# Optimization experiments

Hardware: AMD Instinct MI355X
Metric: run time of the kernel (lower is better)

The kernel has to match this reference:

```python
import jax, jax.numpy as jnp
import numpy as np

SAMPLING_RATE = 48000
HARMONIC_NUM = 8
DIM = HARMONIC_NUM + 1
SINE_AMP = 0.1
NOISE_STD = 0.003
VOICED_THRESHOLD = 0.0


def setup_inputs() -> dict:
    key = jax.random.key(0)
    B, T = 4, 480000
    # realistic voiced pitch contour in [80, 400) Hz
    f0 = jax.random.uniform(key, (B, T, 1), dtype=jnp.float32, minval=80.0, maxval=400.0)
    return {"f0": f0}


def reference(f0):
    B, T, _ = f0.shape
    # harmonic stack: f0_buf[:, :, k] = f0 * (k+1)   -> [B, T, DIM]
    harmonics = jnp.arange(1, DIM + 1, dtype=f0.dtype)
    f0_buf = f0 * harmonics  # broadcast [B,T,1] * [DIM]

    # normalized phase increment per sample
    rad_values = (f0_buf / SAMPLING_RATE) % 1.0

    # random initial phase per (batch, harmonic); fundamental gets phase 0
    k_ini, k_noise = jax.random.split(jax.random.key(42))
    rand_ini = jax.random.uniform(k_ini, (B, DIM), dtype=f0.dtype)
    rand_ini = rand_ini.at[:, 0].set(0.0)
    rad_values = rad_values.at[:, 0, :].add(rand_ini)

    # phase-unwrap correction: detect wrap points of cumsum % 1 and subtract 1
    tmp_over_one = jnp.cumsum(rad_values, axis=1) % 1.0
    wrap = (tmp_over_one[:, 1:, :] - tmp_over_one[:, :-1, :]) < 0  # [B,T-1,DIM]
    cumsum_shift = jnp.concatenate(
        [jnp.zeros((B, 1, DIM), dtype=f0.dtype), -wrap.astype(f0.dtype)], axis=1
    )

    phase = jnp.cumsum(rad_values + cumsum_shift, axis=1) * (2.0 * jnp.pi)
    sine_waves = jnp.sin(phase) * SINE_AMP  # [B,T,DIM]

    # voiced/unvoiced mask from fundamental f0
    uv = (f0 > VOICED_THRESHOLD).astype(f0.dtype)  # [B,T,1]

    noise_amp = uv * NOISE_STD + (1.0 - uv) * (SINE_AMP / 3.0)
    noise = jax.random.normal(k_noise, sine_waves.shape, dtype=f0.dtype)
    return sine_waves * uv + noise_amp * noise
```

## Files before the change

kernel.cpp:

```cpp
#include <hip/hip_runtime.h>
#include <math.h>
#include <stdint.h>

#pragma clang fp contract(off)

#define BB   4
#define TT   480000
#define DIM  9
#define TILE 256
#define NTT  1875

#define PARTITIONABLE 1

__host__ __device__ static inline void threefry2x32(uint32_t k0, uint32_t k1,
                                                    uint32_t x0, uint32_t x1,
                                                    uint32_t& o0, uint32_t& o1) {
  const uint32_t ks2 = k0 ^ k1 ^ 0x1BD11BDAu;
  x0 += k0; x1 += k1;
#define TF_R(r) { x0 += x1; x1 = (x1 << (r)) | (x1 >> (32 - (r))); x1 ^= x0; }
  TF_R(13) TF_R(15) TF_R(26) TF_R(6)
  x0 += k1;  x1 += ks2 + 1u;
  TF_R(17) TF_R(29) TF_R(16) TF_R(24)
  x0 += ks2; x1 += k0 + 2u;
  TF_R(13) TF_R(15) TF_R(26) TF_R(6)
  x0 += k0;  x1 += k1 + 3u;
  TF_R(17) TF_R(29) TF_R(16) TF_R(24)
  x0 += k1;  x1 += ks2 + 4u;
  TF_R(13) TF_R(15) TF_R(26) TF_R(6)
  x0 += ks2; x1 += k0 + 5u;
#undef TF_R
  o0 = x0; o1 = x1;
}

__device__ __forceinline__ float fracf_(float x) { return x - truncf(x); }

__device__ __forceinline__ float u01_(uint32_t bits) {
  return __uint_as_float((bits >> 9) | 0x3f800000u) - 1.0f;
}

__device__ static inline float erfinv_xla(float x) {
  float t = (1.0f - x) * (1.0f + x);
  float w = -0.6931471805599453f * __builtin_amdgcn_logf(t);
  float p;
  if (w < 5.0f) {
    w = w - 2.5f;
    p = 2.81022636e-08f;
    p = 3.43273939e-07f  + p * w;
    p = -3.5233877e-06f  + p * w;
    p = -4.39150654e-06f + p * w;
    p = 0.00021858087f   + p * w;
    p = -0.00125372503f  + p * w;
    p = -0.00417768164f  + p * w;
    p = 0.246640727f     + p * w;
    p = 1.50140941f      + p * w;
  } else {
    w = __builtin_amdgcn_sqrtf(w) - 3.0f;
    p = -0.000200214257f;
    p = 0.000100950558f  + p * w;
    p = 0.00134934322f   + p * w;
    p = -0.00367342844f  + p * w;
    p = 0.00573950773f   + p * w;
    p = -0.0076224613f   + p * w;
    p = 0.00943887047f   + p * w;
    p = 1.00167406f      + p * w;
    p = 2.83297682f      + p * w;
  }
  return p * x;
}

__device__ __forceinline__ float nrm_(uint32_t bits) {
  const float LO = -0.9999999403953552f;
  float u = u01_(bits) * 2.0f + LO;
  u = fmaxf(LO, u);
  return 1.4142135623730951f * erfinv_xla(u);
}

__device__ __forceinline__ uint32_t ri_bits(uint32_t kk0, uint32_t kk1, uint32_t j) {
  uint32_t o0, o1;
#if PARTITIONABLE
  threefry2x32(kk0, kk1, 0u, j, o0, o1);
  return o0 ^ o1;
#else
  if (j < 18u) { threefry2x32(kk0, kk1, j, j + 18u, o0, o1); return o0; }
  threefry2x32(kk0, kk1, j - 18u, j, o0, o1); return o1;
#endif
}

__device__ __forceinline__ uint32_t noise_bits(uint32_t kn0, uint32_t kn1, uint32_t i) {
  uint32_t o0, o1;
#if PARTITIONABLE
  threefry2x32(kn0, kn1, 0u, i, o0, o1);
  return o0 ^ o1;
#else
  const uint32_t half = 2u * TT * DIM;
  if (i < half) { threefry2x32(kn0, kn1, i, i + half, o0, o1); return o0; }
  threefry2x32(kn0, kn1, i - half, i, o0, o1); return o1;
#endif
}

__device__ __forceinline__ float rand_ini_val(uint32_t ki0, uint32_t ki1, int b, int k) {
  if (k == 0) return 0.0f;
  return u01_(ri_bits(ki0, ki1, (uint32_t)(b * DIM + k)));
}

__device__ __forceinline__ float selbit(unsigned long long m, float aFalse, float bTrue) {
  float r;
  asm("v_cndmask_b32 %0, %1, %2, %3" : "=v"(r) : "v"(aFalse), "v"(bTrue), "s"(m));
  return r;
}

struct Tree { float n1a, n1b, Mv[6]; };

__device__ __forceinline__ void build_tree4(float x0, float x1, float x2, float x3,
                                            Tree& T, int l) {
  T.n1a = x0 + x1;
  T.n1b = x2 + x3;
  T.Mv[0] = T.n1a + T.n1b;
#pragma unroll
  for (int s = 1; s < 6; ++s)
    T.Mv[s] = __shfl(T.Mv[s - 1], 2 * l) + __shfl(T.Mv[s - 1], 2 * l + 1);
}
__device__ __forceinline__ float tile_sum4(const Tree& T) {
  return __shfl(T.Mv[5], 0) + __shfl(T.Mv[5], 1);
}
__device__ __forceinline__ float fold4(const Tree& T, int n, float carry) {
  float acc = carry;
#pragma unroll
  for (int b = 7; b >= 2; --b) {
    float t = __shfl(T.Mv[b - 2], (n >> (b + 1)) << 1);
    acc = ((n >> b) & 1) ? acc + t : acc;
  }
  if (n & 2) acc = acc + T.n1a;
  return acc;
}

__global__ __launch_bounds__(256) void k_up1(const float* __restrict__ f0,
                                             float* __restrict__ gL,
                                             uint32_t ki0, uint32_t ki1) {
  int task = blockIdx.x * 4 + (threadIdx.x >> 6);
  int l = threadIdx.x & 63;
  int b = task / NTT, j = task - b * NTT;
  float4 f4 = *(const float4*)(f0 + (size_t)b * TT + j * TILE + 4 * l);
  const float RINV = 1.0f / 48000.0f;
  float rb0 = f4.x * RINV, rb1 = f4.y * RINV, rb2 = f4.z * RINV, rb3 = f4.w * RINV;
  bool ini = (j == 0) & (l == 0);
#pragma unroll
  for (int k = 0; k < DIM; ++k) {
    float h = (float)(k + 1);
    float r0 = fracf_(rb0 * h), r1 = fracf_(rb1 * h);
    float r2 = fracf_(rb2 * h), r3 = fracf_(rb3 * h);
    if (ini) r0 = r0 + rand_ini_val(ki0, ki1, b, k);
    Tree T; build_tree4(r0, r1, r2, r3, T, l);
    float ts = tile_sum4(T);
    if (l == 0) gL[(b * DIM + k) * NTT + j] = ts;
  }
}

__global__ __launch_bounds__(256) void k_midscan(float* __restrict__ gbuf) {
  const int NLEV = 11;
  const int SZ[11]  = {1875, 937, 468, 234, 117, 58, 29, 14, 7, 3, 1};
  const int OFF[11] = {0, 1875, 2812, 3280, 3514, 3631, 3689, 3718, 3732, 3739, 3742};
  __shared__ float buf[4][3743];
  int w = threadIdx.x >> 6, l = threadIdx.x & 63;
  int row = blockIdx.x * 4 + w;
  float* g = gbuf + (size_t)row * NTT;
  float* s = buf[w];
  for (int i = l; i < NTT; i += 64) s[i] = g[i];
#pragma unroll
  for (int lv = 0; lv + 1 < NLEV; ++lv) {
    int m = SZ[lv + 1];
    const float* src = s + OFF[lv];
    float* dst = s + OFF[lv + 1];
    for (int i = l; i < m; i += 64) dst[i] = src[2 * i] + src[2 * i + 1];
  }
#pragma unroll
  for (int lv = NLEV - 2; lv >= 0; --lv) {
    int n = SZ[lv], m = SZ[lv + 1];
    float* cur = s + OFF[lv];
    const float* up = s + OFF[lv + 1];
    for (int i = l; i < m; i += 64) {
      float ss = up[i];
      cur[2 * i + 1] = ss;
      if (2 * i + 2 < n) cur[2 * i + 2] = ss + cur[2 * i + 2];
    }
  }
  for (int i = l; i < NTT; i += 64) g[i] = s[i];
}

__global__ __launch_bounds__(256) void k_d1u2(const float* __restrict__ f0,
                                              const float* __restrict__ gS1,
                                              float* __restrict__ gL2,
                                              ulonglong2* __restrict__ wrapw,
                                              uint32_t ki0, uint32_t ki1) {
  int task = blockIdx.x * 4 + (threadIdx.x >> 6);
  int l = threadIdx.x & 63;
  int b = task / NTT, j = task - b * NTT;
  float4 f4 = *(const float4*)(f0 + (size_t)b * TT + j * TILE + 4 * l);
  const float RINV = 1.0f / 48000.0f;
  float rb0 = f4.x * RINV, rb1 = f4.y * RINV, rb2 = f4.z * RINV, rb3 = f4.w * RINV;
  bool ini = (j == 0) & (l == 0);
  bool notfirst = (j > 0) | (l > 0);
#pragma unroll
  for (int k = 0; k < DIM; ++k) {
    float h = (float)(k + 1);
    float r0 = fracf_(rb0 * h), r1 = fracf_(rb1 * h);
    float r2 = fracf_(rb2 * h), r3 = fracf_(rb3 * h);
    if (ini) r0 = r0 + rand_ini_val(ki0, ki1, b, k);
    Tree T; build_tree4(r0, r1, r2, r3, T, l);
    int bju = __builtin_amdgcn_readfirstlane((b * DIM + k) * NTT + j);
    float S = gS1[bju];
    float C = (j > 0) ? gS1[bju - 1] : 0.0f;
    float c3 = fold4(T, 4 * l + 4, C);
    c3 = (l == 63) ? S : c3;
    float c1 = fold4(T, 4 * l + 2, C);
    float cp = __shfl_up(c3, 1);
    if (l == 0) cp = C;
    float c0 = cp + r0;
    float c2 = c1 + r2;
    float fp = fracf_(cp), g0 = fracf_(c0), g1 = fracf_(c1);
    float g2 = fracf_(c2), g3 = fracf_(c3);
    bool w0 = notfirst & (g0 < fp);
    bool w1 = g1 < g0;
    bool w2 = g2 < g1;
    bool w3 = g3 < g2;
    float y0 = w0 ? r0 - 1.0f : r0, y1 = w1 ? r1 - 1.0f : r1;
    float y2 = w2 ? r2 - 1.0f : r2, y3 = w3 ? r3 - 1.0f : r3;
    unsigned long long m0 = __ballot(w0), m1 = __ballot(w1);
    unsigned long long m2 = __ballot(w2), m3 = __ballot(w3);
    Tree Ty; build_tree4(y0, y1, y2, y3, Ty, l);
    float ts = tile_sum4(Ty);
    if (l == 0) {
      gL2[bju] = ts;
      wrapw[2 * (size_t)bju]     = make_ulonglong2(m0, m1);
      wrapw[2 * (size_t)bju + 1] = make_ulonglong2(m2, m3);
    }
  }
}

__global__ __launch_bounds__(256) void k_d2out(const float* __restrict__ f0,
                                               const float* __restrict__ gS2,
                                               const ulonglong2* __restrict__ wrapw,
                                               float* __restrict__ out,
                                               uint32_t ki0, uint32_t ki1,
                                               uint32_t kn0, uint32_t kn1) {
  __shared__ float sb[4][64 * 37];
  int w = threadIdx.x >> 6, l = threadIdx.x & 63;
  int task = blockIdx.x * 4 + w;
  int b = task / NTT, j = task - b * NTT;
  int t0 = j * TILE + 4 * l;
  float4 f4 = *(const float4*)(f0 + (size_t)b * TT + t0);
  const float RINV = 1.0f / 48000.0f;
  float rb0 = f4.x * RINV, rb1 = f4.y * RINV, rb2 = f4.z * RINV, rb3 = f4.w * RINV;
  bool ini = (j == 0) & (l == 0);
  float uv0 = (f4.x > 0.0f) ? 1.0f : 0.0f, uv1 = (f4.y > 0.0f) ? 1.0f : 0.0f;
  float uv2 = (f4.z > 0.0f) ? 1.0f : 0.0f, uv3 = (f4.w > 0.0f) ? 1.0f : 0.0f;
  const float AMP3 = 0.0333333333333333333f;
  float na0 = uv0 * 0.003f + (1.0f - uv0) * AMP3;
  float na1 = uv1 * 0.003f + (1.0f - uv1) * AMP3;
  float na2 = uv2 * 0.003f + (1.0f - uv2) * AMP3;
  float na3 = uv3 * 0.003f + (1.0f - uv3) * AMP3;
  float* sl = sb[w];
  int sbase = l * 37;
#pragma unroll
  for (int k = 0; k < DIM; ++k) {
    float h = (float)(k + 1);
    float r0 = fracf_(rb0 * h), r1 = fracf_(rb1 * h);
    float r2 = fracf_(rb2 * h), r3 = fracf_(rb3 * h);
    if (ini) r0 = r0 + rand_ini_val(ki0, ki1, b, k);
    int bju = __builtin_amdgcn_readfirstlane((b * DIM + k) * NTT + j);
    ulonglong2 wA = wrapw[2 * (size_t)bju];
    ulonglong2 wB = wrapw[2 * (size_t)bju + 1];
    float S2 = gS2[bju];
    float C2 = (j > 0) ? gS2[bju - 1] : 0.0f;
    float y0 = selbit(wA.x, r0, r0 - 1.0f);
    float y1 = selbit(wA.y, r1, r1 - 1.0f);
    float y2 = selbit(wB.x, r2, r2 - 1.0f);
    float y3 = selbit(wB.y, r3, r3 - 1.0f);
    Tree T; build_tree4(y0, y1, y2, y3, T, l);
    float d3 = fold4(T, 4 * l + 4, C2);
    d3 = (l == 63) ? S2 : d3;
    float d1 = fold4(T, 4 * l + 2, C2);
    float dp = __shfl_up(d3, 1);
    if (l == 0) dp = C2;
    float d0 = dp + y0;
    float d2 = d1 + y2;
    float s0 = __builtin_amdgcn_sinf(d0) * 0.1f;
    float s1 = __builtin_amdgcn_sinf(d1) * 0.1f;
    float s2 = __builtin_amdgcn_sinf(d2) * 0.1f;
    float s3 = __builtin_amdgcn_sinf(d3) * 0.1f;
    uint32_t fi = (uint32_t)(b * TT + t0) * (uint32_t)DIM + (uint32_t)k;
    float n0 = nrm_(noise_bits(kn0, kn1, fi));
    float n1 = nrm_(noise_bits(kn0, kn1, fi + 9u));
    float n2 = nrm_(noise_bits(kn0, kn1, fi + 18u));
    float n3 = nrm_(noise_bits(kn0, kn1, fi + 27u));
    sl[sbase + k]      = s0 * uv0 + na0 * n0;
    sl[sbase + 9 + k]  = s1 * uv1 + na1 * n1;
    sl[sbase + 18 + k] = s2 * uv2 + na2 * n2;
    sl[sbase + 27 + k] = s3 * uv3 + na3 * n3;
  }
  float4* po = (float4*)(out + ((size_t)b * TT + (size_t)j * TILE) * DIM);
#pragma unroll
  for (int q = 0; q < 9; ++q) {
    int gg = (q * 64 + l) * 4;
    int a = gg + gg / 36;
    float4 v = make_float4(sl[a], sl[a + 1], sl[a + 2], sl[a + 3]);
    po[q * 64 + l] = v;
  }
}

extern "C" void kernel_launch(void* const* d_in, const int* in_sizes, int n_in,
                              void* d_out, int out_size, void* d_ws, size_t ws_size,
                              hipStream_t stream) {
  (void)in_sizes; (void)n_in; (void)out_size; (void)ws_size;
  const float* f0 = (const float*)d_in[0];
  float* out = (float*)d_out;
  float* gBuf1 = (float*)d_ws;
  float* gBuf2 = gBuf1 + 36 * NTT;
  ulonglong2* wrapw =
      (ulonglong2*)((char*)d_ws + (size_t)2 * 36 * NTT * sizeof(float));

  uint32_t ki0, ki1, kn0, kn1;
#if PARTITIONABLE
  threefry2x32(0u, 42u, 0u, 0u, ki0, ki1);
  threefry2x32(0u, 42u, 0u, 1u, kn0, kn1);
#else
  uint32_t a0, a1, b0, b1;
  threefry2x32(0u, 42u, 0u, 2u, a0, a1);
  threefry2x32(0u, 42u, 1u, 3u, b0, b1);
  ki0 = a0; ki1 = b0;
  kn0 = a1; kn1 = b1;
#endif

  k_up1    <<<(BB * NTT) / 4, 256, 0, stream>>>(f0, gBuf1, ki0, ki1);
  k_midscan<<<9, 256, 0, stream>>>(gBuf1);
  k_d1u2   <<<(BB * NTT) / 4, 256, 0, stream>>>(f0, gBuf1, gBuf2, wrapw, ki0, ki1);
  k_midscan<<<9, 256, 0, stream>>>(gBuf2);
  k_d2out  <<<(BB * NTT) / 4, 256, 0, stream>>>(f0, gBuf2, wrapw, out,
                                                ki0, ki1, kn0, kn1);
}
```

Baseline: 179.3 us.

## Parallelize midscan across 36 blocks and cache per-lane prefix sums for output pass

The middle scan kernel now uses one 256-thread block per row (36 blocks) instead of one wavefront per row in 9 blocks, with block-wide barriers between tree levels. The second downsweep kernel also stores each lane's inclusive partial sum to a workspace buffer. A new output kernel reads those sums instead of rebuilding the tree and folding the prefix. This trades extra global memory traffic (64 floats per tile per harmonic) for less recomputation, and only runs if the workspace is large enough.

```diff
diff --git a/kernel.cpp b/kernel.cpp
--- a/kernel.cpp
+++ b/kernel.cpp
@@ -160,37 +160,44 @@
   const int NLEV = 11;
   const int SZ[11]  = {1875, 937, 468, 234, 117, 58, 29, 14, 7, 3, 1};
   const int OFF[11] = {0, 1875, 2812, 3280, 3514, 3631, 3689, 3718, 3732, 3739, 3742};
-  __shared__ float buf[4][3743];
-  int w = threadIdx.x >> 6, l = threadIdx.x & 63;
-  int row = blockIdx.x * 4 + w;
-  float* g = gbuf + (size_t)row * NTT;
-  float* s = buf[w];
-  for (int i = l; i < NTT; i += 64) s[i] = g[i];
+  __shared__ float buf[3743];
+  float* g = gbuf + (size_t)blockIdx.x * NTT;
+  int tid = threadIdx.x;
+  float tmp[8];
+#pragma unroll
+  for (int u = 0; u < 8; ++u) { int i = tid + u * 256; tmp[u] = (i < NTT) ? g[i] : 0.0f; }
+#pragma unroll
+  for (int u = 0; u < 8; ++u) { int i = tid + u * 256; if (i < NTT) buf[i] = tmp[u]; }
+  __syncthreads();
 #pragma unroll
   for (int lv = 0; lv + 1 < NLEV; ++lv) {
     int m = SZ[lv + 1];
-    const float* src = s + OFF[lv];
-    float* dst = s + OFF[lv + 1];
-    for (int i = l; i < m; i += 64) dst[i] = src[2 * i] + src[2 * i + 1];
+    const float* src = buf + OFF[lv];
+    float* dst = buf + OFF[lv + 1];
+    for (int i = tid; i < m; i += 256) dst[i] = src[2 * i] + src[2 * i + 1];
+    __syncthreads();
   }
 #pragma unroll
   for (int lv = NLEV - 2; lv >= 0; --lv) {
     int n = SZ[lv], m = SZ[lv + 1];
-    float* cur = s + OFF[lv];
-    const float* up = s + OFF[lv + 1];
-    for (int i = l; i < m; i += 64) {
-      float ss = up[i];
-      cur[2 * i + 1] = ss;
-      if (2 * i + 2 < n) cur[2 * i + 2] = ss + cur[2 * i + 2];
+    float* cur = buf + OFF[lv];
+    const float* up = buf + OFF[lv + 1];
+    for (int i = tid; i < m; i += 256) {
+      float s = up[i];
+      cur[2 * i + 1] = s;
+      if (2 * i + 2 < n) cur[2 * i + 2] = s + cur[2 * i + 2];
     }
-  }
-  for (int i = l; i < NTT; i += 64) g[i] = s[i];
+    __syncthreads();
+  }
+#pragma unroll
+  for (int u = 0; u < 8; ++u) { int i = tid + u * 256; if (i < NTT) g[i] = buf[i]; }
 }
 
 __global__ __launch_bounds__(256) void k_d1u2(const float* __restrict__ f0,
                                               const float* __restrict__ gS1,
                                               float* __restrict__ gL2,
                                               ulonglong2* __restrict__ wrapw,
+                                              float* __restrict__ q0buf, int useq,
                                               uint32_t ki0, uint32_t ki1) {
   int task = blockIdx.x * 4 + (threadIdx.x >> 6);
   int l = threadIdx.x & 63;
@@ -229,11 +236,83 @@
     unsigned long long m2 = __ballot(w2), m3 = __ballot(w3);
     Tree Ty; build_tree4(y0, y1, y2, y3, Ty, l);
     float ts = tile_sum4(Ty);
+    if (useq) {
+      float q0 = (l == 63) ? ts : fold4(Ty, 4 * l + 4, 0.0f);
+      q0buf[(size_t)bju * 64 + l] = q0;
+    }
     if (l == 0) {
       gL2[bju] = ts;
       wrapw[2 * (size_t)bju]     = make_ulonglong2(m0, m1);
       wrapw[2 * (size_t)bju + 1] = make_ulonglong2(m2, m3);
     }
+  }
+}
+
+__global__ __launch_bounds__(256) void k_d2out_q(const float* __restrict__ f0,
+                                                 const float* __restrict__ gS2,
+                                                 const ulonglong2* __restrict__ wrapw,
+                                                 const float* __restrict__ q0buf,
+                                                 float* __restrict__ out,
+                                                 uint32_t ki0, uint32_t ki1,
+                                                 uint32_t kn0, uint32_t kn1) {
+  __shared__ float sb[4][64 * 37];
+  int w = threadIdx.x >> 6, l = threadIdx.x & 63;
+  int task = blockIdx.x * 4 + w;
+  int b = task / NTT, j = task - b * NTT;
+  int t0 = j * TILE + 4 * l;
+  float4 f4 = *(const float4*)(f0 + (size_t)b * TT + t0);
+  const float RINV = 1.0f / 48000.0f;
+  float rb0 = f4.x * RINV, rb1 = f4.y * RINV, rb2 = f4.z * RINV;
+  bool ini = (j == 0) & (l == 0);
+  float uv0 = (f4.x > 0.0f) ? 1.0f : 0.0f, uv1 = (f4.y > 0.0f) ? 1.0f : 0.0f;
+  float uv2 = (f4.z > 0.0f) ? 1.0f : 0.0f, uv3 = (f4.w > 0.0f) ? 1.0f : 0.0f;
+  const float AMP3 = 0.0333333333333333333f;
+  float na0 = uv0 * 0.003f + (1.0f - uv0) * AMP3;
+  float na1 = uv1 * 0.003f + (1.0f - uv1) * AMP3;
+  float na2 = uv2 * 0.003f + (1.0f - uv2) * AMP3;
+  float na3 = uv3 * 0.003f + (1.0f - uv3) * AMP3;
+  float* sl = sb[w];
+  int sbase = l * 37;
+#pragma unroll
+  for (int k = 0; k < DIM; ++k) {
+    float h = (float)(k + 1);
+    float r0 = fracf_(rb0 * h), r1 = fracf_(rb1 * h), r2 = fracf_(rb2 * h);
+    if (ini) r0 = r0 + rand_ini_val(ki0, ki1, b, k);
+    int bju = __builtin_amdgcn_readfirstlane((b * DIM + k) * NTT + j);
+    ulonglong2 wA = wrapw[2 * (size_t)bju];
+    unsigned long long wBx = wrapw[2 * (size_t)bju + 1].x;
+    float C2 = (j > 0) ? gS2[bju - 1] : 0.0f;
+    float qv = q0buf[(size_t)bju * 64 + l];
+    float qp = __shfl_up(qv, 1);
+    if (l == 0) qp = 0.0f;
+    float y0 = selbit(wA.x, r0, r0 - 1.0f);
+    float y1 = selbit(wA.y, r1, r1 - 1.0f);
+    float y2 = selbit(wBx, r2, r2 - 1.0f);
+    float base = C2 + qp;
+    float d0 = base + y0;
+    float d1 = base + (y0 + y1);
+    float d2 = d1 + y2;
+    float d3 = C2 + qv;
+    float s0 = __builtin_amdgcn_sinf(d0) * 0.1f;
+    float s1 = __builtin_amdgcn_sinf(d1) * 0.1f;
+    float s2 = __builtin_amdgcn_sinf(d2) * 0.1f;
+    float s3 = __builtin_amdgcn_sinf(d3) * 0.1f;
+    uint32_t fi = (uint32_t)(b * TT + t0) * (uint32_t)DIM + (uint32_t)k;
+    float n0 = nrm_(noise_bits(kn0, kn1, fi));
+    float n1 = nrm_(noise_bits(kn0, kn1, fi + 9u));
+    float n2 = nrm_(noise_bits(kn0, kn1, fi + 18u));
+    float n3 = nrm_(noise_bits(kn0, kn1, fi + 27u));
+    sl[sbase + k]      = s0 * uv0 + na0 * n0;
+    sl[sbase + 9 + k]  = s1 * uv1 + na1 * n1;
+    sl[sbase + 18 + k] = s2 * uv2 + na2 * n2;
+    sl[sbase + 27 + k] = s3 * uv3 + na3 * n3;
+  }
+  float4* po = (float4*)(out + ((size_t)b * TT + (size_t)j * TILE) * DIM);
+#pragma unroll
+  for (int q = 0; q < 9; ++q) {
+    int gg = (q * 64 + l) * 4;
+    int a = gg + gg / 36;
+    po[q * 64 + l] = make_float4(sl[a], sl[a + 1], sl[a + 2], sl[a + 3]);
   }
 }
 
@@ -303,21 +382,25 @@
   for (int q = 0; q < 9; ++q) {
     int gg = (q * 64 + l) * 4;
     int a = gg + gg / 36;
-    float4 v = make_float4(sl[a], sl[a + 1], sl[a + 2], sl[a + 3]);
-    po[q * 64 + l] = v;
+    po[q * 64 + l] = make_float4(sl[a], sl[a + 1], sl[a + 2], sl[a + 3]);
   }
 }
 
 extern "C" void kernel_launch(void* const* d_in, const int* in_sizes, int n_in,
                               void* d_out, int out_size, void* d_ws, size_t ws_size,
                               hipStream_t stream) {
-  (void)in_sizes; (void)n_in; (void)out_size; (void)ws_size;
+  (void)in_sizes; (void)n_in; (void)out_size;
   const float* f0 = (const float*)d_in[0];
   float* out = (float*)d_out;
+  const size_t LANES = (size_t)BB * DIM;
   float* gBuf1 = (float*)d_ws;
-  float* gBuf2 = gBuf1 + 36 * NTT;
+  float* gBuf2 = gBuf1 + LANES * NTT;
   ulonglong2* wrapw =
-      (ulonglong2*)((char*)d_ws + (size_t)2 * 36 * NTT * sizeof(float));
+      (ulonglong2*)((char*)d_ws + 2 * LANES * NTT * sizeof(float));
+  size_t baseBytes = 2 * LANES * NTT * sizeof(float) + LANES * NTT * 32;
+  size_t qBytes = LANES * NTT * 64 * sizeof(float);
+  float* q0buf = (float*)((char*)d_ws + baseBytes);
+  int useq = (ws_size >= baseBytes + qBytes) ? 1 : 0;
 
   uint32_t ki0, ki1, kn0, kn1;
 #if PARTITIONABLE
@@ -332,9 +415,14 @@
 #endif
 
   k_up1    <<<(BB * NTT) / 4, 256, 0, stream>>>(f0, gBuf1, ki0, ki1);
-  k_midscan<<<9, 256, 0, stream>>>(gBuf1);
-  k_d1u2   <<<(BB * NTT) / 4, 256, 0, stream>>>(f0, gBuf1, gBuf2, wrapw, ki0, ki1);
-  k_midscan<<<9, 256, 0, stream>>>(gBuf2);
-  k_d2out  <<<(BB * NTT) / 4, 256, 0, stream>>>(f0, gBuf2, wrapw, out,
-                                                ki0, ki1, kn0, kn1);
-}
+  k_midscan<<<36, 256, 0, stream>>>(gBuf1);
+  k_d1u2   <<<(BB * NTT) / 4, 256, 0, stream>>>(f0, gBuf1, gBuf2, wrapw,
+                                                q0buf, useq, ki0, ki1);
+  k_midscan<<<36, 256, 0, stream>>>(gBuf2);
+  if (useq)
+    k_d2out_q<<<(BB * NTT) / 4, 256, 0, stream>>>(f0, gBuf2, wrapw, q0buf, out,
+                                                  ki0, ki1, kn0, kn1);
+  else
+    k_d2out  <<<(BB * NTT) / 4, 256, 0, stream>>>(f0, gBuf2, wrapw, out,
+                                                  ki0, ki1, kn0, kn1);
+}
```

Measured after the change: 173.4 us. -3.3%, faster.
